# Performance work log

Hardware: AMD Instinct MI355X
Metric: run time of the kernel (lower is better)

The kernel has to match this reference:

```python
import jax, jax.numpy as jnp
import numpy as np

B, C, IN_F = 8, 1024, 256
NH, OF = 8, 128  # num_heads, out_features
TEMP = 1.5
LN_EPS = 1e-5


def setup_inputs() -> dict:
    key = jax.random.key(0)
    ks = jax.random.split(key, 8)
    H = jax.random.normal(ks[0], (B, C, IN_F), dtype=jnp.float32)
    A = jax.random.uniform(ks[1], (B, C, C), dtype=jnp.float32)
    W = jax.random.normal(ks[2], (IN_F, NH * OF), dtype=jnp.float32) * 0.05
    a = jax.random.normal(ks[3], (NH, 2 * OF), dtype=jnp.float32) * 0.05
    res_W = jax.random.normal(ks[4], (IN_F, NH * OF), dtype=jnp.float32) * 0.05
    res_b = jnp.zeros((NH * OF,), dtype=jnp.float32)
    ln_gamma = jnp.ones((NH * OF,), dtype=jnp.float32)
    ln_beta = jnp.zeros((NH * OF,), dtype=jnp.float32)
    return {"H": H, "A": A, "W": W, "a": a, "res_W": res_W,
            "res_b": res_b, "ln_gamma": ln_gamma, "ln_beta": ln_beta}


def reference(H, A, W, a, res_W, res_b, ln_gamma, ln_beta):
    b, c, _ = H.shape
    # Wh: [B, C, H, F]
    Wh = (H @ W).reshape(b, c, NH, OF)
    # Split attention vector a = [a_src | a_dst] so that
    # einsum('bijhf,hf', cat(Wh_i, Wh_j), a) == e_src[i] + e_dst[j]
    a_src, a_dst = a[:, :OF], a[:, OF:]
    e_src = jnp.einsum('bchf,hf->bch', Wh, a_src)  # [B, C, H]
    e_dst = jnp.einsum('bchf,hf->bch', Wh, a_dst)  # [B, C, H]
    e = e_src[:, :, None, :] + e_dst[:, None, :, :]  # [B, C, C, H]
    e = jnp.where(e > 0, e, 0.2 * e)  # LeakyReLU(0.2)
    # adjacency mask with self-loops
    mask = (A > 0) | jnp.eye(c, dtype=bool)[None]  # [B, C, C]
    e = jnp.where(mask[..., None], e, -1e9)
    # row-normalized adjacency as additive bias
    A_norm = A / (A.sum(axis=-1, keepdims=True) + 1e-8)
    e = e + A_norm[..., None]
    alpha = jax.nn.softmax(e / TEMP, axis=2)  # softmax over j (dim=2)
    # dropout disabled (inference / p-effective 0)
    H_out = jnp.einsum('bijh,bjhf->bihf', alpha, Wh).reshape(b, c, NH * OF)
    x = H_out + (H @ res_W + res_b)
    mu = x.mean(axis=-1, keepdims=True)
    var = x.var(axis=-1, keepdims=True)
    x = (x - mu) * jax.lax.rsqrt(var + LN_EPS) * ln_gamma + ln_beta
    return jax.nn.relu(x), alpha
```

## Files before the change

### kernel.cpp

```cpp
#include <hip/hip_runtime.h>

#define BB 8
#define CC 1024
#define FF 256
#define NHH 8
#define OFF 128
#define NHOF 1024
#define KSCALE 0.9617966939259756f

typedef __attribute__((ext_vector_type(8))) short s8v;
typedef __attribute__((ext_vector_type(4))) short s4v;
typedef __attribute__((ext_vector_type(2))) short s2v;
typedef __attribute__((ext_vector_type(4))) float f32x4;
typedef __attribute__((ext_vector_type(16))) float f32x16;

__device__ __forceinline__ ushort f2b(float f) {
  union { float f; uint u; } v; v.f = f;
  uint r = v.u + 0x7FFFu + ((v.u >> 16) & 1u);
  return (ushort)(r >> 16);
}

__global__ __launch_bounds__(256) void k_prep(const float* __restrict__ W,
    const float* __restrict__ RW, short* __restrict__ Wt, short* __restrict__ RWt)
{
  __shared__ float st[32][33];
  const float* src = blockIdx.z ? RW : W;
  short* dst = blockIdx.z ? RWt : Wt;
  const int n0 = blockIdx.x * 32, k0 = blockIdx.y * 32;
  const int t = threadIdx.x;
  {
    int kr = t >> 3, nq = (t & 7) * 4;
    float4 v = *reinterpret_cast<const float4*>(src + (size_t)(k0 + kr) * NHOF + n0 + nq);
    st[kr][nq] = v.x; st[kr][nq + 1] = v.y; st[kr][nq + 2] = v.z; st[kr][nq + 3] = v.w;
  }
  __syncthreads();
  {
    int nr = t >> 3, kq = (t & 7) * 4;
    s4v pk;
    pk[0] = (short)f2b(st[kq + 0][nr]); pk[1] = (short)f2b(st[kq + 1][nr]);
    pk[2] = (short)f2b(st[kq + 2][nr]); pk[3] = (short)f2b(st[kq + 3][nr]);
    *reinterpret_cast<s4v*>(dst + (size_t)(n0 + nr) * FF + k0 + kq) = pk;
  }
}

__global__ __launch_bounds__(256) void k_gemm(const float* __restrict__ H,
    const short* __restrict__ Wt, const short* __restrict__ RWt,
    const float* __restrict__ rb, const float* __restrict__ att,
    short* __restrict__ WhT, float* __restrict__ Rs,
    float* __restrict__ esg, float* __restrict__ edg)
{
  __shared__ short As[128 * 32];
  __shared__ short Bs[128 * 32];
  __shared__ float ep[2][128][2];
  const int t = threadIdx.x, l = t & 63, w = t >> 6;
  const int wr = w >> 1, wc = w & 1;
  const int nb = blockIdx.x, m0 = blockIdx.y * 128;
  const bool isW = nb < 8;
  const int n0 = (nb & 7) * 128;
  const short* Bg = isW ? Wt : RWt;

  f32x4 acc[4][4];
#pragma unroll
  for (int mi = 0; mi < 4; ++mi)
#pragma unroll
    for (int ni = 0; ni < 4; ++ni)
#pragma unroll
      for (int r = 0; r < 4; ++r) acc[mi][ni][r] = 0.f;

  const int srow = t >> 1, skh = (t & 1) * 16;
  const float* hsrc = H + (size_t)(m0 + srow) * FF + skh;
  const short* bsrc = Bg + (size_t)(n0 + srow) * FF + skh;
  const int fr = l & 15, kg = (l >> 4) * 8;

  for (int k0 = 0; k0 < FF; k0 += 32) {
    float4 h0 = *reinterpret_cast<const float4*>(hsrc + k0);
    float4 h1 = *reinterpret_cast<const float4*>(hsrc + k0 + 4);
    float4 h2 = *reinterpret_cast<const float4*>(hsrc + k0 + 8);
    float4 h3 = *reinterpret_cast<const float4*>(hsrc + k0 + 12);
    s8v b0 = *reinterpret_cast<const s8v*>(bsrc + k0);
    s8v b1 = *reinterpret_cast<const s8v*>(bsrc + k0 + 8);
    s8v p0, p1;
    p0[0] = (short)f2b(h0.x); p0[1] = (short)f2b(h0.y); p0[2] = (short)f2b(h0.z); p0[3] = (short)f2b(h0.w);
    p0[4] = (short)f2b(h1.x); p0[5] = (short)f2b(h1.y); p0[6] = (short)f2b(h1.z); p0[7] = (short)f2b(h1.w);
    p1[0] = (short)f2b(h2.x); p1[1] = (short)f2b(h2.y); p1[2] = (short)f2b(h2.z); p1[3] = (short)f2b(h2.w);
    p1[4] = (short)f2b(h3.x); p1[5] = (short)f2b(h3.y); p1[6] = (short)f2b(h3.z); p1[7] = (short)f2b(h3.w);
    *reinterpret_cast<s8v*>(As + srow * 32 + skh) = p0;
    *reinterpret_cast<s8v*>(As + srow * 32 + skh + 8) = p1;
    *reinterpret_cast<s8v*>(Bs + srow * 32 + skh) = b0;
    *reinterpret_cast<s8v*>(Bs + srow * 32 + skh + 8) = b1;
    __syncthreads();
    s8v aF[4], bF[4];
#pragma unroll
    for (int mi = 0; mi < 4; ++mi)
      aF[mi] = *reinterpret_cast<const s8v*>(As + (wr * 64 + mi * 16 + fr) * 32 + kg);
#pragma unroll
    for (int ni = 0; ni < 4; ++ni)
      bF[ni] = *reinterpret_cast<const s8v*>(Bs + (wc * 64 + ni * 16 + fr) * 32 + kg);
#pragma unroll
    for (int mi = 0; mi < 4; ++mi)
#pragma unroll
      for (int ni = 0; ni < 4; ++ni)
        acc[mi][ni] = __builtin_amdgcn_mfma_f32_16x16x32_bf16(aF[mi], bF[ni], acc[mi][ni], 0, 0, 0);
    __syncthreads();
  }

  const int bb = m0 >> 10, jl0 = m0 & 1023;
  if (isW) {
    const int h = nb;
#pragma unroll
    for (int mi = 0; mi < 4; ++mi)
#pragma unroll
      for (int ni = 0; ni < 4; ++ni) {
        int f = wc * 64 + ni * 16 + (l & 15);
        int j = jl0 + wr * 64 + mi * 16 + (l >> 4) * 4;
        s4v pk;
        pk[0] = (short)f2b(acc[mi][ni][0]); pk[1] = (short)f2b(acc[mi][ni][1]);
        pk[2] = (short)f2b(acc[mi][ni][2]); pk[3] = (short)f2b(acc[mi][ni][3]);
        *reinterpret_cast<s4v*>(WhT + (size_t)((bb * 8 + h) * 128 + f) * 1024 + j) = pk;
      }
    float aS[4], aD[4];
#pragma unroll
    for (int ni = 0; ni < 4; ++ni) {
      int f = wc * 64 + ni * 16 + (l & 15);
      aS[ni] = att[h * 256 + f];
      aD[ni] = att[h * 256 + 128 + f];
    }
#pragma unroll
    for (int mi = 0; mi < 4; ++mi)
#pragma unroll
      for (int r = 0; r < 4; ++r) {
        float ps = acc[mi][0][r] * aS[0] + acc[mi][1][r] * aS[1] + acc[mi][2][r] * aS[2] + acc[mi][3][r] * aS[3];
        float pd = acc[mi][0][r] * aD[0] + acc[mi][1][r] * aD[1] + acc[mi][2][r] * aD[2] + acc[mi][3][r] * aD[3];
#pragma unroll
        for (int m = 1; m <= 8; m <<= 1) { ps += __shfl_xor(ps, m); pd += __shfl_xor(pd, m); }
        if ((l & 15) == 0) {
          int row = wr * 64 + mi * 16 + (l >> 4) * 4 + r;
          ep[wc][row][0] = ps; ep[wc][row][1] = pd;
        }
      }
    __syncthreads();
    {
      int row = t >> 1, sel = t & 1;
      float v = ep[0][row][sel] + ep[1][row][sel];
      float* dst = sel ? edg : esg;
      dst[(size_t)((bb << 10) + jl0 + row) * 8 + h] = v;
    }
  } else {
#pragma unroll
    for (int mi = 0; mi < 4; ++mi)
#pragma unroll
      for (int ni = 0; ni < 4; ++ni) {
        int n = n0 + wc * 64 + ni * 16 + (l & 15);
        float bias = rb[n];
        int m = m0 + wr * 64 + mi * 16 + (l >> 4) * 4;
#pragma unroll
        for (int r = 0; r < 4; ++r)
          Rs[(size_t)(m + r) * NHOF + n] = acc[mi][ni][r] + bias;
      }
  }
}

__global__ __launch_bounds__(256, 2) void k_attn(const float* __restrict__ A,
    const short* __restrict__ WhT, const float* __restrict__ esg,
    const float* __restrict__ edg, float* __restrict__ alp, float* __restrict__ ho)
{
  __shared__ short WhS[1024 * 16];
  __shared__ float edK[8 * 1028];
  __shared__ short alS[8 * 32 * 16];
  __shared__ float esK[32 * 8];
  __shared__ float liS[32 * 8];
  __shared__ float rsS[32];

  const int t = threadIdx.x, l = t & 63, w = t >> 6;
  const int b = blockIdx.x >> 5, i0 = (blockIdx.x & 31) << 5;

#pragma unroll
  for (int c = 0; c < 32; ++c) {
    int idx = t + c * 256;
    int j = idx >> 3, h = idx & 7;
    edK[h * 1028 + j] = edg[(size_t)b * 8192 + idx] * KSCALE;
  }
  {
    int i = t >> 3, h = t & 7;
    esK[t] = esg[(size_t)((b << 10) + i0 + i) * 8 + h] * KSCALE;
  }

  {
    int i = w * 8 + (l >> 3), jsub = l & 7;
    const float* Ar = A + (size_t)((b << 10) + i0 + i) * 1024;
    float s = 0.f;
#pragma unroll
    for (int c = 0; c < 32; ++c) {
      float4 v = *reinterpret_cast<const float4*>(Ar + jsub * 4 + c * 32);
      s += v.x + v.y + v.z + v.w;
    }
    s += __shfl_xor(s, 1); s += __shfl_xor(s, 2); s += __shfl_xor(s, 4);
    if (jsub == 0) rsS[i] = 1.f / (s + 1e-8f);
  }
  __syncthreads();

  {
    const int i = t >> 3, jsub = t & 7, ig = i0 + i;
    const float* Ar = A + (size_t)((b << 10) + ig) * 1024;
    const float rs = rsS[i];
    float eK[8];
#pragma unroll
    for (int h = 0; h < 8; ++h) eK[h] = esK[i * 8 + h];
    float lac[8] = {0, 0, 0, 0, 0, 0, 0, 0};
    for (int jq = 0; jq < 32; ++jq) {
      int j = jq * 32 + jsub * 4;
      float4 av4 = *reinterpret_cast<const float4*>(Ar + j);
      float ea0 = (av4.x > 0.f || (j + 0) == ig) ? exp2f(av4.x * rs * KSCALE) : 0.f;
      float ea1 = (av4.y > 0.f || (j + 1) == ig) ? exp2f(av4.y * rs * KSCALE) : 0.f;
      float ea2 = (av4.z > 0.f || (j + 2) == ig) ? exp2f(av4.z * rs * KSCALE) : 0.f;
      float ea3 = (av4.w > 0.f || (j + 3) == ig) ? exp2f(av4.w * rs * KSCALE) : 0.f;
#pragma unroll
      for (int h = 0; h < 8; ++h) {
        const float* ed4 = edK + h * 1028 + j;
        float s0 = eK[h] + ed4[0]; s0 = fmaxf(s0, 0.2f * s0);
        float s1 = eK[h] + ed4[1]; s1 = fmaxf(s1, 0.2f * s1);
        float s2 = eK[h] + ed4[2]; s2 = fmaxf(s2, 0.2f * s2);
        float s3 = eK[h] + ed4[3]; s3 = fmaxf(s3, 0.2f * s3);
        lac[h] = fmaf(exp2f(s0), ea0, lac[h]);
        lac[h] = fmaf(exp2f(s1), ea1, lac[h]);
        lac[h] = fmaf(exp2f(s2), ea2, lac[h]);
        lac[h] = fmaf(exp2f(s3), ea3, lac[h]);
      }
    }
#pragma unroll
    for (int h = 0; h < 8; ++h) {
      float v = lac[h];
      v += __shfl_xor(v, 1); v += __shfl_xor(v, 2); v += __shfl_xor(v, 4);
      if (jsub == 0) liS[i * 8 + h] = 1.f / v;
    }
  }
  __syncthreads();

  const int h0 = w * 2;
  f32x16 acc[2][4];
#pragma unroll
  for (int hh = 0; hh < 2; ++hh)
#pragma unroll
    for (int ff = 0; ff < 4; ++ff)
#pragma unroll
      for (int r = 0; r < 16; ++r) acc[hh][ff][r] = 0.f;

  const int i_p = t >> 3, jp = (t & 7) * 2, igP = i0 + i_p;
  const float rsP = rsS[i_p];
  float eKP[8], liP[8];
#pragma unroll
  for (int h = 0; h < 8; ++h) { eKP[h] = esK[i_p * 8 + h]; liP[h] = liS[i_p * 8 + h]; }
  const float* ArP = A + (size_t)((b << 10) + igP) * 1024;
  const short* Whb = WhT + (size_t)b * 1048576;

  for (int j0 = 0; j0 < 1024; j0 += 16) {
    s8v sreg[8];
#pragma unroll
    for (int c = 0; c < 4; ++c) {
      const short* src = Whb + (size_t)(t + c * 256) * 1024 + j0;
      sreg[c * 2] = *reinterpret_cast<const s8v*>(src);
      sreg[c * 2 + 1] = *reinterpret_cast<const s8v*>(src + 8);
    }
    float2 a2 = *reinterpret_cast<const float2*>(ArP + j0 + jp);
    float alo[2][8];
#pragma unroll
    for (int e = 0; e < 2; ++e) {
      float aij = e ? a2.y : a2.x;
      int j = j0 + jp + e;
      float ea = (aij > 0.f || j == igP) ? exp2f(aij * rsP * KSCALE) : 0.f;
#pragma unroll
      for (int h = 0; h < 8; ++h) {
        float s = eKP[h] + edK[h * 1028 + j];
        s = fmaxf(s, 0.2f * s);
        alo[e][h] = exp2f(s) * ea * liP[h];
      }
    }
    float* ap = alp + (size_t)((b << 10) + igP) * 8192 + (size_t)(j0 + jp) * 8;
    *reinterpret_cast<float4*>(ap)      = make_float4(alo[0][0], alo[0][1], alo[0][2], alo[0][3]);
    *reinterpret_cast<float4*>(ap + 4)  = make_float4(alo[0][4], alo[0][5], alo[0][6], alo[0][7]);
    *reinterpret_cast<float4*>(ap + 8)  = make_float4(alo[1][0], alo[1][1], alo[1][2], alo[1][3]);
    *reinterpret_cast<float4*>(ap + 12) = make_float4(alo[1][4], alo[1][5], alo[1][6], alo[1][7]);
#pragma unroll
    for (int h = 0; h < 8; ++h) {
      s2v pk; pk[0] = (short)f2b(alo[0][h]); pk[1] = (short)f2b(alo[1][h]);
      *reinterpret_cast<s2v*>(alS + h * 512 + i_p * 16 + jp) = pk;
    }
#pragma unroll
    for (int c = 0; c < 4; ++c) {
      *reinterpret_cast<s8v*>(WhS + (t + c * 256) * 16) = sreg[c * 2];
      *reinterpret_cast<s8v*>(WhS + (t + c * 256) * 16 + 8) = sreg[c * 2 + 1];
    }
    __syncthreads();
#pragma unroll
    for (int hh = 0; hh < 2; ++hh) {
      int h = h0 + hh;
      s8v af = *reinterpret_cast<const s8v*>(alS + h * 512 + (l & 31) * 16 + (l >> 5) * 8);
#pragma unroll
      for (int ff = 0; ff < 4; ++ff) {
        s8v bf = *reinterpret_cast<const s8v*>(WhS + (h * 128 + ff * 32 + (l & 31)) * 16 + (l >> 5) * 8);
        acc[hh][ff] = __builtin_amdgcn_mfma_f32_32x32x16_bf16(af, bf, acc[hh][ff], 0, 0, 0);
      }
    }
    __syncthreads();
  }

#pragma unroll
  for (int hh = 0; hh < 2; ++hh)
#pragma unroll
    for (int ff = 0; ff < 4; ++ff) {
      int f = ff * 32 + (l & 31);
      float* op = ho + (size_t)((b << 10) + i0) * 1024 + (h0 + hh) * 128 + f;
#pragma unroll
      for (int reg = 0; reg < 16; ++reg) {
        int irow = (reg & 3) + 8 * (reg >> 2) + 4 * (l >> 5);
        op[(size_t)irow * 1024] = acc[hh][ff][reg];
      }
    }
}

__global__ __launch_bounds__(256) void k_ln(const float* __restrict__ Rs,
    const float* __restrict__ g, const float* __restrict__ bt, float* __restrict__ out)
{
  __shared__ float sm[8];
  const int row = blockIdx.x;
  const int t = threadIdx.x;
  size_t base = (size_t)row * NHOF + t * 4;
  float4 hv = *reinterpret_cast<const float4*>(out + base);
  float4 rv = *reinterpret_cast<const float4*>(Rs + base);
  float x0 = hv.x + rv.x, x1 = hv.y + rv.y, x2 = hv.z + rv.z, x3 = hv.w + rv.w;
  float s  = x0 + x1 + x2 + x3;
  float ss = x0 * x0 + x1 * x1 + x2 * x2 + x3 * x3;
#pragma unroll
  for (int m = 32; m; m >>= 1) { s += __shfl_xor(s, m); ss += __shfl_xor(ss, m); }
  if ((t & 63) == 0) { sm[t >> 6] = s; sm[4 + (t >> 6)] = ss; }
  __syncthreads();
  s  = sm[0] + sm[1] + sm[2] + sm[3];
  ss = sm[4] + sm[5] + sm[6] + sm[7];
  float mu = s * (1.f / 1024.f);
  float var = ss * (1.f / 1024.f) - mu * mu;
  float rstd = rsqrtf(var + 1e-5f);
  float4 gv = *reinterpret_cast<const float4*>(g + t * 4);
  float4 bv = *reinterpret_cast<const float4*>(bt + t * 4);
  float y0 = fmaxf((x0 - mu) * rstd * gv.x + bv.x, 0.f);
  float y1 = fmaxf((x1 - mu) * rstd * gv.y + bv.y, 0.f);
  float y2 = fmaxf((x2 - mu) * rstd * gv.z + bv.z, 0.f);
  float y3 = fmaxf((x3 - mu) * rstd * gv.w + bv.w, 0.f);
  *reinterpret_cast<float4*>(out + base) = make_float4(y0, y1, y2, y3);
}

extern "C" void kernel_launch(void* const* d_in, const int* in_sizes, int n_in,
                              void* d_out, int out_size, void* d_ws, size_t ws_size,
                              hipStream_t stream) {
  const float* H    = (const float*)d_in[0];
  const float* A    = (const float*)d_in[1];
  const float* W    = (const float*)d_in[2];
  const float* av   = (const float*)d_in[3];
  const float* resW = (const float*)d_in[4];
  const float* resb = (const float*)d_in[5];
  const float* gam  = (const float*)d_in[6];
  const float* bet  = (const float*)d_in[7];

  float* out0  = (float*)d_out;
  float* alpha = out0 + (size_t)BB * CC * NHOF;

  short* WhT = (short*)d_ws;
  float* res = (float*)(WhT + (size_t)8388608);
  float* esg = res + (size_t)8388608;
  float* edg = esg + 65536;
  short* Wtb = (short*)(edg + 65536);
  short* RWtb = Wtb + 262144;

  k_prep<<<dim3(32, 8, 2), 256, 0, stream>>>(W, resW, Wtb, RWtb);
  k_gemm<<<dim3(16, 64), 256, 0, stream>>>(H, Wtb, RWtb, resb, av, WhT, res, esg, edg);
  k_attn<<<256, 256, 0, stream>>>(A, WhT, esg, edg, alpha, out0);
  k_ln  <<<BB * CC, 256, 0, stream>>>(res, gam, bet, out0);
}
```

Before: 527.2 us.

## Restructure attention kernel to 1024 threads with double-buffered alpha tiles and direct Wh loads

Measured after the change: 484.0 us. 8.2% less time.

```diff
diff --git a/kernel.cpp b/kernel.cpp
--- a/kernel.cpp
+++ b/kernel.cpp
@@ -10,7 +10,6 @@
 
 typedef __attribute__((ext_vector_type(8))) short s8v;
 typedef __attribute__((ext_vector_type(4))) short s4v;
-typedef __attribute__((ext_vector_type(2))) short s2v;
 typedef __attribute__((ext_vector_type(4))) float f32x4;
 typedef __attribute__((ext_vector_type(16))) float f32x16;
 
@@ -49,9 +48,10 @@
     short* __restrict__ WhT, float* __restrict__ Rs,
     float* __restrict__ esg, float* __restrict__ edg)
 {
-  __shared__ short As[128 * 32];
-  __shared__ short Bs[128 * 32];
+  __shared__ short SU[8192];
   __shared__ float ep[2][128][2];
+  short* As = SU;
+  short* Bs = SU + 4096;
   const int t = threadIdx.x, l = t & 63, w = t >> 6;
   const int wr = w >> 1, wc = w & 1;
   const int nb = blockIdx.x, m0 = blockIdx.y * 128;
@@ -107,17 +107,6 @@
   const int bb = m0 >> 10, jl0 = m0 & 1023;
   if (isW) {
     const int h = nb;
-#pragma unroll
-    for (int mi = 0; mi < 4; ++mi)
-#pragma unroll
-      for (int ni = 0; ni < 4; ++ni) {
-        int f = wc * 64 + ni * 16 + (l & 15);
-        int j = jl0 + wr * 64 + mi * 16 + (l >> 4) * 4;
-        s4v pk;
-        pk[0] = (short)f2b(acc[mi][ni][0]); pk[1] = (short)f2b(acc[mi][ni][1]);
-        pk[2] = (short)f2b(acc[mi][ni][2]); pk[3] = (short)f2b(acc[mi][ni][3]);
-        *reinterpret_cast<s4v*>(WhT + (size_t)((bb * 8 + h) * 128 + f) * 1024 + j) = pk;
-      }
     float aS[4], aD[4];
 #pragma unroll
     for (int ni = 0; ni < 4; ++ni) {
@@ -138,7 +127,34 @@
           ep[wc][row][0] = ps; ep[wc][row][1] = pd;
         }
       }
-    __syncthreads();
+#pragma unroll
+    for (int c = 0; c < 4; ++c) {
+      if (wc == (c >> 1)) {
+        const int nia = (c & 1) * 2;
+#pragma unroll
+        for (int mi = 0; mi < 4; ++mi)
+#pragma unroll
+          for (int nq = 0; nq < 2; ++nq) {
+            const int ni = nia + nq;
+            const int f_loc = nq * 16 + (l & 15);
+            const int jloc = wr * 64 + mi * 16 + (l >> 4) * 4;
+            s4v pk;
+            pk[0] = (short)f2b(acc[mi][ni][0]); pk[1] = (short)f2b(acc[mi][ni][1]);
+            pk[2] = (short)f2b(acc[mi][ni][2]); pk[3] = (short)f2b(acc[mi][ni][3]);
+            *reinterpret_cast<s4v*>(SU + f_loc * 136 + jloc) = pk;
+          }
+      }
+      __syncthreads();
+      {
+        const int f_loc = t >> 3, jq = t & 7;
+        s8v v0 = *reinterpret_cast<const s8v*>(SU + f_loc * 136 + jq * 16);
+        s8v v1 = *reinterpret_cast<const s8v*>(SU + f_loc * 136 + jq * 16 + 8);
+        short* dst = WhT + (size_t)((bb * 8 + h) * 128 + c * 32 + f_loc) * 1024 + jl0 + jq * 16;
+        *reinterpret_cast<s8v*>(dst) = v0;
+        *reinterpret_cast<s8v*>(dst + 8) = v1;
+      }
+      __syncthreads();
+    }
     {
       int row = t >> 1, sel = t & 1;
       float v = ep[0][row][sel] + ep[1][row][sel];
@@ -160,13 +176,12 @@
   }
 }
 
-__global__ __launch_bounds__(256, 2) void k_attn(const float* __restrict__ A,
+__global__ __launch_bounds__(1024) void k_attn(const float* __restrict__ A,
     const short* __restrict__ WhT, const float* __restrict__ esg,
     const float* __restrict__ edg, float* __restrict__ alp, float* __restrict__ ho)
 {
-  __shared__ short WhS[1024 * 16];
-  __shared__ float edK[8 * 1028];
-  __shared__ short alS[8 * 32 * 16];
+  __shared__ short alSf[2 * 8 * 32 * 32];
+  __shared__ float edKT[1024 * 8];
   __shared__ float esK[32 * 8];
   __shared__ float liS[32 * 8];
   __shared__ float rsS[32];
@@ -175,147 +190,141 @@
   const int b = blockIdx.x >> 5, i0 = (blockIdx.x & 31) << 5;
 
 #pragma unroll
-  for (int c = 0; c < 32; ++c) {
-    int idx = t + c * 256;
-    int j = idx >> 3, h = idx & 7;
-    edK[h * 1028 + j] = edg[(size_t)b * 8192 + idx] * KSCALE;
-  }
-  {
-    int i = t >> 3, h = t & 7;
-    esK[t] = esg[(size_t)((b << 10) + i0 + i) * 8 + h] * KSCALE;
-  }
-
-  {
-    int i = w * 8 + (l >> 3), jsub = l & 7;
-    const float* Ar = A + (size_t)((b << 10) + i0 + i) * 1024;
+  for (int c = 0; c < 8; ++c) {
+    int idx = t + c * 1024;
+    edKT[idx] = edg[(size_t)b * 8192 + idx] * KSCALE;
+  }
+  if (t < 256) esK[t] = esg[(size_t)((b << 10) + i0 + (t >> 3)) * 8 + (t & 7)] * KSCALE;
+
+  const int i = t >> 5, jsub = t & 31;
+  const float* Ar = A + (size_t)((b << 10) + i0 + i) * 1024;
+
+  {
     float s = 0.f;
 #pragma unroll
-    for (int c = 0; c < 32; ++c) {
-      float4 v = *reinterpret_cast<const float4*>(Ar + jsub * 4 + c * 32);
+    for (int c = 0; c < 8; ++c) {
+      float4 v = *reinterpret_cast<const float4*>(Ar + jsub * 4 + c * 128);
       s += v.x + v.y + v.z + v.w;
     }
     s += __shfl_xor(s, 1); s += __shfl_xor(s, 2); s += __shfl_xor(s, 4);
+    s += __shfl_xor(s, 8); s += __shfl_xor(s, 16);
     if (jsub == 0) rsS[i] = 1.f / (s + 1e-8f);
   }
   __syncthreads();
 
   {
-    const int i = t >> 3, jsub = t & 7, ig = i0 + i;
-    const float* Ar = A + (size_t)((b << 10) + ig) * 1024;
+    const int ig = i0 + i;
     const float rs = rsS[i];
     float eK[8];
 #pragma unroll
-    for (int h = 0; h < 8; ++h) eK[h] = esK[i * 8 + h];
-    float lac[8] = {0, 0, 0, 0, 0, 0, 0, 0};
-    for (int jq = 0; jq < 32; ++jq) {
-      int j = jq * 32 + jsub * 4;
-      float4 av4 = *reinterpret_cast<const float4*>(Ar + j);
-      float ea0 = (av4.x > 0.f || (j + 0) == ig) ? exp2f(av4.x * rs * KSCALE) : 0.f;
-      float ea1 = (av4.y > 0.f || (j + 1) == ig) ? exp2f(av4.y * rs * KSCALE) : 0.f;
-      float ea2 = (av4.z > 0.f || (j + 2) == ig) ? exp2f(av4.z * rs * KSCALE) : 0.f;
-      float ea3 = (av4.w > 0.f || (j + 3) == ig) ? exp2f(av4.w * rs * KSCALE) : 0.f;
-#pragma unroll
-      for (int h = 0; h < 8; ++h) {
-        const float* ed4 = edK + h * 1028 + j;
-        float s0 = eK[h] + ed4[0]; s0 = fmaxf(s0, 0.2f * s0);
-        float s1 = eK[h] + ed4[1]; s1 = fmaxf(s1, 0.2f * s1);
-        float s2 = eK[h] + ed4[2]; s2 = fmaxf(s2, 0.2f * s2);
-        float s3 = eK[h] + ed4[3]; s3 = fmaxf(s3, 0.2f * s3);
-        lac[h] = fmaf(exp2f(s0), ea0, lac[h]);
-        lac[h] = fmaf(exp2f(s1), ea1, lac[h]);
-        lac[h] = fmaf(exp2f(s2), ea2, lac[h]);
-        lac[h] = fmaf(exp2f(s3), ea3, lac[h]);
-      }
-    }
-#pragma unroll
-    for (int h = 0; h < 8; ++h) {
-      float v = lac[h];
+    for (int h2 = 0; h2 < 8; ++h2) eK[h2] = esK[i * 8 + h2];
+    float lac = 0.f;
+    float lach[8] = {0, 0, 0, 0, 0, 0, 0, 0};
+    (void)lac;
+    for (int jj = 0; jj < 32; ++jj) {
+      int j = jsub + jj * 32;
+      float aij = Ar[j];
+      float ea = (aij > 0.f || j == ig) ? exp2f(aij * rs * KSCALE) : 0.f;
+      float4 e0 = *reinterpret_cast<const float4*>(edKT + j * 8);
+      float4 e1 = *reinterpret_cast<const float4*>(edKT + j * 8 + 4);
+      float ed[8] = {e0.x, e0.y, e0.z, e0.w, e1.x, e1.y, e1.z, e1.w};
+#pragma unroll
+      for (int h2 = 0; h2 < 8; ++h2) {
+        float s = eK[h2] + ed[h2];
+        s = fmaxf(s, 0.2f * s);
+        lach[h2] = fmaf(exp2f(s), ea, lach[h2]);
+      }
+    }
+#pragma unroll
+    for (int h2 = 0; h2 < 8; ++h2) {
+      float v = lach[h2];
       v += __shfl_xor(v, 1); v += __shfl_xor(v, 2); v += __shfl_xor(v, 4);
-      if (jsub == 0) liS[i * 8 + h] = 1.f / v;
+      v += __shfl_xor(v, 8); v += __shfl_xor(v, 16);
+      if (jsub == 0) liS[i * 8 + h2] = 1.f / v;
     }
   }
   __syncthreads();
 
-  const int h0 = w * 2;
-  f32x16 acc[2][4];
-#pragma unroll
-  for (int hh = 0; hh < 2; ++hh)
-#pragma unroll
-    for (int ff = 0; ff < 4; ++ff)
-#pragma unroll
-      for (int r = 0; r < 16; ++r) acc[hh][ff][r] = 0.f;
-
-  const int i_p = t >> 3, jp = (t & 7) * 2, igP = i0 + i_p;
-  const float rsP = rsS[i_p];
+  const int ip = i, jp = jsub, igP = i0 + ip;
+  const float rsP = rsS[ip];
   float eKP[8], liP[8];
 #pragma unroll
-  for (int h = 0; h < 8; ++h) { eKP[h] = esK[i_p * 8 + h]; liP[h] = liS[i_p * 8 + h]; }
-  const float* ArP = A + (size_t)((b << 10) + igP) * 1024;
-  const short* Whb = WhT + (size_t)b * 1048576;
-
-  for (int j0 = 0; j0 < 1024; j0 += 16) {
-    s8v sreg[8];
-#pragma unroll
-    for (int c = 0; c < 4; ++c) {
-      const short* src = Whb + (size_t)(t + c * 256) * 1024 + j0;
-      sreg[c * 2] = *reinterpret_cast<const s8v*>(src);
-      sreg[c * 2 + 1] = *reinterpret_cast<const s8v*>(src + 8);
-    }
-    float2 a2 = *reinterpret_cast<const float2*>(ArP + j0 + jp);
-    float alo[2][8];
-#pragma unroll
-    for (int e = 0; e < 2; ++e) {
-      float aij = e ? a2.y : a2.x;
-      int j = j0 + jp + e;
+  for (int h2 = 0; h2 < 8; ++h2) { eKP[h2] = esK[ip * 8 + h2]; liP[h2] = liS[ip * 8 + h2]; }
+  const float* ArP = Ar;
+  const int hM = w >> 1, fh = w & 1;
+  const short* Wb = WhT + ((size_t)(b * 8 + hM) << 17) + (size_t)(fh * 64 + (l & 31)) * 1024 + (l >> 5) * 8;
+  f32x16 acc0, acc1;
+#pragma unroll
+  for (int r = 0; r < 16; ++r) { acc0[r] = 0.f; acc1[r] = 0.f; }
+
+  float areg[8];
+  {
+    const int j = jp;
+    float aij = ArP[j];
+    float ea = (aij > 0.f || j == igP) ? exp2f(aij * rsP * KSCALE) : 0.f;
+    float4 e0 = *reinterpret_cast<const float4*>(edKT + j * 8);
+    float4 e1 = *reinterpret_cast<const float4*>(edKT + j * 8 + 4);
+    float ed[8] = {e0.x, e0.y, e0.z, e0.w, e1.x, e1.y, e1.z, e1.w};
+#pragma unroll
+    for (int h2 = 0; h2 < 8; ++h2) {
+      float s = eKP[h2] + ed[h2];
+      s = fmaxf(s, 0.2f * s);
+      areg[h2] = exp2f(s) * ea * liP[h2];
+    }
+    float* ap = alp + (size_t)((b << 10) + igP) * 8192 + (size_t)j * 8;
+    *reinterpret_cast<float4*>(ap)     = make_float4(areg[0], areg[1], areg[2], areg[3]);
+    *reinterpret_cast<float4*>(ap + 4) = make_float4(areg[4], areg[5], areg[6], areg[7]);
+  }
+
+  const int swW = ((jp >> 3) ^ (ip & 3)) << 3;
+  const int swR = (l & 31) & 3;
+  for (int k = 0; k < 32; ++k) {
+    const int buf = k & 1;
+    {
+      short* as = alSf + buf * 8192 + ip * 32 + swW + (jp & 7);
+#pragma unroll
+      for (int h2 = 0; h2 < 8; ++h2) as[h2 * 1024] = (short)f2b(areg[h2]);
+    }
+    __syncthreads();
+    s8v bf00 = *reinterpret_cast<const s8v*>(Wb + k * 32);
+    s8v bf01 = *reinterpret_cast<const s8v*>(Wb + k * 32 + 16);
+    s8v bf10 = *reinterpret_cast<const s8v*>(Wb + 32768 + k * 32);
+    s8v bf11 = *reinterpret_cast<const s8v*>(Wb + 32768 + k * 32 + 16);
+    if (k < 31) {
+      const int j = (k + 1) * 32 + jp;
+      float aij = ArP[j];
       float ea = (aij > 0.f || j == igP) ? exp2f(aij * rsP * KSCALE) : 0.f;
-#pragma unroll
-      for (int h = 0; h < 8; ++h) {
-        float s = eKP[h] + edK[h * 1028 + j];
+      float4 e0 = *reinterpret_cast<const float4*>(edKT + j * 8);
+      float4 e1 = *reinterpret_cast<const float4*>(edKT + j * 8 + 4);
+      float ed[8] = {e0.x, e0.y, e0.z, e0.w, e1.x, e1.y, e1.z, e1.w};
+#pragma unroll
+      for (int h2 = 0; h2 < 8; ++h2) {
+        float s = eKP[h2] + ed[h2];
         s = fmaxf(s, 0.2f * s);
-        alo[e][h] = exp2f(s) * ea * liP[h];
-      }
-    }
-    float* ap = alp + (size_t)((b << 10) + igP) * 8192 + (size_t)(j0 + jp) * 8;
-    *reinterpret_cast<float4*>(ap)      = make_float4(alo[0][0], alo[0][1], alo[0][2], alo[0][3]);
-    *reinterpret_cast<float4*>(ap + 4)  = make_float4(alo[0][4], alo[0][5], alo[0][6], alo[0][7]);
-    *reinterpret_cast<float4*>(ap + 8)  = make_float4(alo[1][0], alo[1][1], alo[1][2], alo[1][3]);
-    *reinterpret_cast<float4*>(ap + 12) = make_float4(alo[1][4], alo[1][5], alo[1][6], alo[1][7]);
-#pragma unroll
-    for (int h = 0; h < 8; ++h) {
-      s2v pk; pk[0] = (short)f2b(alo[0][h]); pk[1] = (short)f2b(alo[1][h]);
-      *reinterpret_cast<s2v*>(alS + h * 512 + i_p * 16 + jp) = pk;
-    }
-#pragma unroll
-    for (int c = 0; c < 4; ++c) {
-      *reinterpret_cast<s8v*>(WhS + (t + c * 256) * 16) = sreg[c * 2];
-      *reinterpret_cast<s8v*>(WhS + (t + c * 256) * 16 + 8) = sreg[c * 2 + 1];
-    }
-    __syncthreads();
-#pragma unroll
-    for (int hh = 0; hh < 2; ++hh) {
-      int h = h0 + hh;
-      s8v af = *reinterpret_cast<const s8v*>(alS + h * 512 + (l & 31) * 16 + (l >> 5) * 8);
-#pragma unroll
-      for (int ff = 0; ff < 4; ++ff) {
-        s8v bf = *reinterpret_cast<const s8v*>(WhS + (h * 128 + ff * 32 + (l & 31)) * 16 + (l >> 5) * 8);
-        acc[hh][ff] = __builtin_amdgcn_mfma_f32_32x32x16_bf16(af, bf, acc[hh][ff], 0, 0, 0);
-      }
-    }
-    __syncthreads();
-  }
-
-#pragma unroll
-  for (int hh = 0; hh < 2; ++hh)
-#pragma unroll
-    for (int ff = 0; ff < 4; ++ff) {
-      int f = ff * 32 + (l & 31);
-      float* op = ho + (size_t)((b << 10) + i0) * 1024 + (h0 + hh) * 128 + f;
-#pragma unroll
-      for (int reg = 0; reg < 16; ++reg) {
-        int irow = (reg & 3) + 8 * (reg >> 2) + 4 * (l >> 5);
-        op[(size_t)irow * 1024] = acc[hh][ff][reg];
-      }
-    }
+        areg[h2] = exp2f(s) * ea * liP[h2];
+      }
+      float* ap = alp + (size_t)((b << 10) + igP) * 8192 + (size_t)j * 8;
+      *reinterpret_cast<float4*>(ap)     = make_float4(areg[0], areg[1], areg[2], areg[3]);
+      *reinterpret_cast<float4*>(ap + 4) = make_float4(areg[4], areg[5], areg[6], areg[7]);
+    }
+    const short* afp = alSf + buf * 8192 + hM * 1024 + (l & 31) * 32;
+    s8v af0 = *reinterpret_cast<const s8v*>(afp + ((((l >> 5)) ^ swR) << 3));
+    s8v af1 = *reinterpret_cast<const s8v*>(afp + (((2 | (l >> 5)) ^ swR) << 3));
+    acc0 = __builtin_amdgcn_mfma_f32_32x32x16_bf16(af0, bf00, acc0, 0, 0, 0);
+    acc0 = __builtin_amdgcn_mfma_f32_32x32x16_bf16(af1, bf01, acc0, 0, 0, 0);
+    acc1 = __builtin_amdgcn_mfma_f32_32x32x16_bf16(af0, bf10, acc1, 0, 0, 0);
+    acc1 = __builtin_amdgcn_mfma_f32_32x32x16_bf16(af1, bf11, acc1, 0, 0, 0);
+  }
+
+  {
+    float* op = ho + (size_t)((b << 10) + i0) * 1024 + hM * 128 + fh * 64 + (l & 31);
+#pragma unroll
+    for (int reg = 0; reg < 16; ++reg) {
+      int irow = (reg & 3) + 8 * (reg >> 2) + 4 * (l >> 5);
+      op[(size_t)irow * 1024]      = acc0[reg];
+      op[(size_t)irow * 1024 + 32] = acc1[reg];
+    }
+  }
 }
 
 __global__ __launch_bounds__(256) void k_ln(const float* __restrict__ Rs,
@@ -372,6 +381,6 @@
 
   k_prep<<<dim3(32, 8, 2), 256, 0, stream>>>(W, resW, Wtb, RWtb);
   k_gemm<<<dim3(16, 64), 256, 0, stream>>>(H, Wtb, RWtb, resb, av, WhT, res, esg, edg);
-  k_attn<<<256, 256, 0, stream>>>(A, WhT, esg, edg, alpha, out0);
+  k_attn<<<256, 1024, 0, stream>>>(A, WhT, esg, edg, alpha, out0);
   k_ln  <<<BB * CC, 256, 0, stream>>>(res, gam, bet, out0);
 }
```
